# Optimization experiments

Measured on AMD Instinct MI355X. Metric: run time of the kernel, lower is better.

## Reference

```python
import jax, jax.numpy as jnp
import numpy as np
import math

B = 131072
D = 256  # latent_dim / emb_dim
MAX_T = 1000
MAX_PERIOD = 10000.0


def timestep_embedding(t, dim):
    # torch: half = dim//2; freqs = exp(-ln(max_period) * arange(half)/half)
    half = dim // 2
    freqs = jnp.exp(-math.log(MAX_PERIOD) * jnp.arange(half, dtype=jnp.float32) / half)
    args = t.astype(jnp.float32)[:, None] * freqs[None, :]  # [B, half]
    emb = jnp.concatenate([jnp.cos(args), jnp.sin(args)], axis=-1)  # [B, dim] (dim even)
    return emb


def setup_inputs() -> dict:
    key = jax.random.key(0)
    ks = jax.random.split(key, 8)
    s_emb = 0.05  # keep activations well-scaled
    x = jax.random.normal(ks[0], (B, D), jnp.float32)
    c = jax.random.normal(ks[1], (B, D), jnp.float32)
    t = jax.random.randint(ks[2], (B,), 0, MAX_T)
    # Linear weights stored torch-style as [out_features, in_features]
    W_step = jax.random.normal(ks[3], (D, D), jnp.float32) * (1.0 / math.sqrt(D))
    b_step = jnp.zeros((D,), jnp.float32)
    W1 = jax.random.normal(ks[4], (3 * D, 3 * D), jnp.float32) * math.sqrt(2.0 / (6 * D))
    b1 = jnp.zeros((3 * D,), jnp.float32)
    W2 = jax.random.normal(ks[5], (D, 3 * D), jnp.float32) * math.sqrt(2.0 / (4 * D))
    b2 = jnp.zeros((3 * D,), jnp.float32)
    del s_emb
    return {"x": x, "c": c, "t": t, "W_step": W_step, "b_step": b_step,
            "W1": W1, "b1": b1, "W2": W2, "b2": b2}


def reference(x, c, t, W_step, b_step, W1, b1, W2, b2):
    # t = step_mlp(timestep_embedding(t, D))
    t_emb = timestep_embedding(t, D) @ W_step.T + b_step           # [B, D]
    model_input = jnp.concatenate([x, c, t_emb], axis=1)           # [B, 3D]
    # diffuser: Linear(3D,3D) -> LeakyReLU(0.01) -> Linear(3D,D)
    h = jax.nn.leaky_relu(model_input @ W1.T + b1, negative_slope=0.01)
    out = h @ W2.T + b2[:D] if b2.shape[0] != D else h @ W2.T + b2
    return out
```

## Files before the change

### kernel.cpp

```cpp
#include <hip/hip_runtime.h>
#include <math.h>

#define DD    256
#define D3    768
#define KXC   512
#define MAXT  1000
#define BM    64
#define NTHR  1024
#define SMEM_BYTES 163840

using s16x8  = __attribute__((ext_vector_type(8))) short;
using f32x16 = __attribute__((ext_vector_type(16))) float;
using u16x4  = __attribute__((ext_vector_type(4))) unsigned short;

__device__ __forceinline__ unsigned short f2bf(float f) {
    union { float f; unsigned u; } v; v.f = f;
    unsigned r = v.u + 0x7fffu + ((v.u >> 16) & 1u);
    return (unsigned short)(r >> 16);
}
__device__ __forceinline__ float bf2f(unsigned short h) {
    union { unsigned u; float f; } v; v.u = ((unsigned)h) << 16;
    return v.f;
}

__global__ void k_temb(const float* __restrict__ Wstep, const float* __restrict__ bstep,
                       float* __restrict__ Temb) {
    __shared__ float emb[DD];
    const int tt  = blockIdx.x;
    const int tid = threadIdx.x;
    if (tid < 128) {
        const float nl = -9.210340371976184f;
        float f = expf(nl * (float)tid / 128.0f);
        float a = (float)tt * f;
        emb[tid]       = cosf(a);
        emb[tid + 128] = sinf(a);
    }
    __syncthreads();
    float acc = bstep[tid];
    const float* wr = Wstep + tid * DD;
    for (int k = 0; k < DD; ++k) acc = fmaf(emb[k], wr[k], acc);
    Temb[tt * DD + tid] = acc;
}

__global__ void k_t1(const float* __restrict__ Temb, const float* __restrict__ W1,
                     const float* __restrict__ b1, float* __restrict__ T1) {
    __shared__ float te[DD];
    const int tt = blockIdx.x;
    const int n  = blockIdx.y * 256 + threadIdx.x;
    te[threadIdx.x] = Temb[tt * DD + threadIdx.x];
    __syncthreads();
    float acc = b1[n];
    const float* wr = W1 + n * D3 + KXC;
    for (int k = 0; k < DD; ++k) acc = fmaf(te[k], wr[k], acc);
    T1[tt * D3 + n] = acc;
}

__global__ void k_cvtW1(const float* __restrict__ W1, unsigned short* __restrict__ hi,
                        unsigned short* __restrict__ lo) {
    int i = blockIdx.x * 256 + threadIdx.x;
    if (i >= 32 * 768 * 16) return;
    int j  = i & 7;
    int h  = (i >> 3) & 1;
    int nn = (i >> 4) % 768;
    int ks = (i >> 4) / 768;
    int k  = ks * 16 + h * 8 + j;
    float v = W1[(size_t)nn * D3 + k];
    unsigned short hh = f2bf(v);
    hi[i] = hh;
    lo[i] = f2bf(v - bf2f(hh));
}

__global__ void k_cvtW2(const float* __restrict__ W2, unsigned short* __restrict__ hi,
                        unsigned short* __restrict__ lo) {
    int i = blockIdx.x * 256 + threadIdx.x;
    if (i >= 48 * 256 * 16) return;
    int j  = i & 7;
    int h  = (i >> 3) & 1;
    int nn = (i >> 4) % 256;
    int kq = (i >> 4) / 256;
    int k  = kq * 16 + h * 8 + j;
    float v = W2[(size_t)nn * D3 + k];
    unsigned short hh = f2bf(v);
    hi[i] = hh;
    lo[i] = f2bf(v - bf2f(hh));
}

__global__ __launch_bounds__(NTHR, 4)
void k_main(const float* __restrict__ x, const float* __restrict__ c,
            const int* __restrict__ t, const float* __restrict__ T1,
            const unsigned short* __restrict__ W1hi, const unsigned short* __restrict__ W1lo,
            const unsigned short* __restrict__ W2hi, const unsigned short* __restrict__ W2lo,
            const float* __restrict__ b2, float* __restrict__ out) {
    extern __shared__ __align__(16) char smem[];
    char* Ah = smem;
    char* Al = smem + 65536;

    const int tid  = threadIdx.x;
    const int lane = tid & 63;
    const int wid  = tid >> 6;
    const int wm   = wid >> 3;
    const int wn   = wid & 7;
    const int l31  = lane & 31;
    const int lh   = lane >> 5;
    const int row0 = blockIdx.x * BM;

    const s16x8* W1hiV = (const s16x8*)W1hi;
    const s16x8* W1loV = (const s16x8*)W1lo;
    const s16x8* W2hiV = (const s16x8*)W2hi;
    const s16x8* W2loV = (const s16x8*)W2lo;

    #pragma unroll
    for (int it = 0; it < 8; ++it) {
        int q    = it * NTHR + tid;
        int row  = q >> 7;
        int col4 = q & 127;
        int k    = col4 * 4;
        const float* src = (k < 256) ? &x[(size_t)(row0 + row) * DD + k]
                                     : &c[(size_t)(row0 + row) * DD + (k - 256)];
        float4 v = *(const float4*)src;
        float f[4] = {v.x, v.y, v.z, v.w};
        u16x4 hv, lv;
        #pragma unroll
        for (int j = 0; j < 4; ++j) {
            unsigned short hh = f2bf(f[j]);
            hv[j] = hh;
            lv[j] = f2bf(f[j] - bf2f(hh));
        }
        int ks = k >> 4, h = (k >> 3) & 1, pos = k & 7;
        char* dst = Ah + ((((ks * 2 + h) * 64) + row) << 4) + pos * 2;
        *(u16x4*)dst = hv;
        *(u16x4*)(dst + 65536) = lv;
    }
    __syncthreads();

    f32x16 oacc;
    #pragma unroll
    for (int r = 0; r < 16; ++r) oacc[r] = 0.f;
    const float b2r = b2[wn * 32 + l31];

    #pragma unroll 1
    for (int p = 0; p < 3; ++p) {
        const int c0 = p * 256 + wn * 32;

        float tv[16];
        #pragma unroll
        for (int r = 0; r < 16; ++r) {
            int m = wm * 32 + (r & 3) + 8 * (r >> 2) + 4 * lh;
            tv[r] = T1[(size_t)t[row0 + m] * D3 + c0 + l31];
        }

        f32x16 acc1;
        #pragma unroll
        for (int r = 0; r < 16; ++r) acc1[r] = 0.f;

        const int nb = c0 + l31;
        const int arow = wm * 32 + l31;

        #pragma unroll 8
        for (int ks = 0; ks < 32; ++ks) {
            const s16x8 ahf = *(const s16x8*)(Ah + ((((ks * 2 + lh) * 64) + arow) << 4));
            const s16x8 alf = *(const s16x8*)(Al + ((((ks * 2 + lh) * 64) + arow) << 4));
            const s16x8 bhf = W1hiV[(ks * D3 + nb) * 2 + lh];
            const s16x8 blf = W1loV[(ks * D3 + nb) * 2 + lh];
            acc1 = __builtin_amdgcn_mfma_f32_32x32x16_bf16(alf, bhf, acc1, 0, 0, 0);
            acc1 = __builtin_amdgcn_mfma_f32_32x32x16_bf16(ahf, blf, acc1, 0, 0, 0);
            acc1 = __builtin_amdgcn_mfma_f32_32x32x16_bf16(ahf, bhf, acc1, 0, 0, 0);
        }

        #pragma unroll 1
        for (int s = 0; s < 4; ++s) {
            char* Hb = smem + 131072 + (s & 1) * 16384;
            if ((wn >> 1) == s) {
                #pragma unroll
                for (int r = 0; r < 16; ++r) {
                    int m = wm * 32 + (r & 3) + 8 * (r >> 2) + 4 * lh;
                    float v = acc1[r] + tv[r];
                    v = v > 0.f ? v : 0.01f * v;
                    unsigned short hh = f2bf(v);
                    unsigned short ll = f2bf(v - bf2f(hh));
                    int cl  = (wn & 1) * 32 + l31;
                    int kl  = cl >> 4, hb = (cl >> 3) & 1, pos = cl & 7;
                    int off = ((((kl * 2 + hb) * 64) + m) << 4) + pos * 2;
                    *(unsigned short*)(Hb + off)        = hh;
                    *(unsigned short*)(Hb + 8192 + off) = ll;
                }
            }
            __syncthreads();
            const int kq0 = p * 16 + s * 4;
            #pragma unroll
            for (int kl = 0; kl < 4; ++kl) {
                int hoff = (((kl * 2 + lh) * 64) + arow) << 4;
                const s16x8 hhf = *(const s16x8*)(Hb + hoff);
                const s16x8 hlf = *(const s16x8*)(Hb + 8192 + hoff);
                int wi = ((kq0 + kl) * DD + wn * 32 + l31) * 2 + lh;
                const s16x8 whf = W2hiV[wi];
                const s16x8 wlf = W2loV[wi];
                oacc = __builtin_amdgcn_mfma_f32_32x32x16_bf16(hlf, whf, oacc, 0, 0, 0);
                oacc = __builtin_amdgcn_mfma_f32_32x32x16_bf16(hhf, wlf, oacc, 0, 0, 0);
                oacc = __builtin_amdgcn_mfma_f32_32x32x16_bf16(hhf, whf, oacc, 0, 0, 0);
            }
        }
    }

    #pragma unroll
    for (int r = 0; r < 16; ++r) {
        int m = wm * 32 + (r & 3) + 8 * (r >> 2) + 4 * lh;
        out[(size_t)(row0 + m) * DD + wn * 32 + l31] = oacc[r] + b2r;
    }
}

extern "C" void kernel_launch(void* const* d_in, const int* in_sizes, int n_in,
                              void* d_out, int out_size, void* d_ws, size_t ws_size,
                              hipStream_t stream) {
    const float* x     = (const float*)d_in[0];
    const float* c     = (const float*)d_in[1];
    const int*   t     = (const int*)  d_in[2];
    const float* Wstep = (const float*)d_in[3];
    const float* bstep = (const float*)d_in[4];
    const float* W1    = (const float*)d_in[5];
    const float* b1    = (const float*)d_in[6];
    const float* W2    = (const float*)d_in[7];
    const float* b2    = (const float*)d_in[8];
    float*       out   = (float*)d_out;

    const int B = in_sizes[0] / DD;

    char* ws = (char*)d_ws;
    float*          Temb = (float*)(ws);
    float*          T1   = (float*)(ws + 1024000);
    unsigned short* W1hi = (unsigned short*)(ws + 4096000);
    unsigned short* W1lo = (unsigned short*)(ws + 4882432);
    unsigned short* W2hi = (unsigned short*)(ws + 5668864);
    unsigned short* W2lo = (unsigned short*)(ws + 6062080);

    k_temb<<<MAXT, 256, 0, stream>>>(Wstep, bstep, Temb);
    k_t1<<<dim3(MAXT, 3), 256, 0, stream>>>(Temb, W1, b1, T1);
    k_cvtW1<<<(32 * 768 * 16 + 255) / 256, 256, 0, stream>>>(W1, W1hi, W1lo);
    k_cvtW2<<<(48 * 256 * 16 + 255) / 256, 256, 0, stream>>>(W2, W2hi, W2lo);

    hipFuncSetAttribute((const void*)k_main, hipFuncAttributeMaxDynamicSharedMemorySize, SMEM_BYTES);
    k_main<<<B / BM, NTHR, SMEM_BYTES, stream>>>(x, c, t, T1, W1hi, W1lo, W2hi, W2lo, b2, out);
}
```

Before: 1.054 ms.

## Replace split-bf16 triple MFMA with single fp16 MFMA and retile main kernel

Drops the hi/lo bf16 split emulation, which needed three MFMAs per tile, and instead uses one fp16 MFMA per tile with fp16 weights, activations and T1 table. The block shrinks to 8 waves, each computing two 32-row M tiles so every B fragment is reused twice. LDS use drops to 80KB, and an XOR swizzle is added to avoid bank conflicts. This cuts MFMA work and memory traffic roughly threefold, at the cost of lower precision: fp16 has about 11 mantissa bits versus roughly 16 for the split scheme, and fp16 can overflow on large activations.

```diff
diff --git a/kernel.cpp b/kernel.cpp
--- a/kernel.cpp
+++ b/kernel.cpp
@@ -6,22 +6,13 @@
 #define KXC   512
 #define MAXT  1000
 #define BM    64
-#define NTHR  1024
-#define SMEM_BYTES 163840
-
-using s16x8  = __attribute__((ext_vector_type(8))) short;
+#define NTHR  512
+#define SMEM_BYTES (65536 + 16384)
+
+typedef _Float16 f16;
+using f16x8  = __attribute__((ext_vector_type(8))) _Float16;
+using f16x4  = __attribute__((ext_vector_type(4))) _Float16;
 using f32x16 = __attribute__((ext_vector_type(16))) float;
-using u16x4  = __attribute__((ext_vector_type(4))) unsigned short;
-
-__device__ __forceinline__ unsigned short f2bf(float f) {
-    union { float f; unsigned u; } v; v.f = f;
-    unsigned r = v.u + 0x7fffu + ((v.u >> 16) & 1u);
-    return (unsigned short)(r >> 16);
-}
-__device__ __forceinline__ float bf2f(unsigned short h) {
-    union { unsigned u; float f; } v; v.u = ((unsigned)h) << 16;
-    return v.f;
-}
 
 __global__ void k_temb(const float* __restrict__ Wstep, const float* __restrict__ bstep,
                        float* __restrict__ Temb) {
@@ -43,7 +34,7 @@
 }
 
 __global__ void k_t1(const float* __restrict__ Temb, const float* __restrict__ W1,
-                     const float* __restrict__ b1, float* __restrict__ T1) {
+                     const float* __restrict__ b1, f16* __restrict__ T1) {
     __shared__ float te[DD];
     const int tt = blockIdx.x;
     const int n  = blockIdx.y * 256 + threadIdx.x;
@@ -52,11 +43,10 @@
     float acc = b1[n];
     const float* wr = W1 + n * D3 + KXC;
     for (int k = 0; k < DD; ++k) acc = fmaf(te[k], wr[k], acc);
-    T1[tt * D3 + n] = acc;
-}
-
-__global__ void k_cvtW1(const float* __restrict__ W1, unsigned short* __restrict__ hi,
-                        unsigned short* __restrict__ lo) {
+    T1[tt * D3 + n] = (f16)acc;
+}
+
+__global__ void k_cvtW1(const float* __restrict__ W1, f16* __restrict__ Wf) {
     int i = blockIdx.x * 256 + threadIdx.x;
     if (i >= 32 * 768 * 16) return;
     int j  = i & 7;
@@ -64,14 +54,10 @@
     int nn = (i >> 4) % 768;
     int ks = (i >> 4) / 768;
     int k  = ks * 16 + h * 8 + j;
-    float v = W1[(size_t)nn * D3 + k];
-    unsigned short hh = f2bf(v);
-    hi[i] = hh;
-    lo[i] = f2bf(v - bf2f(hh));
-}
-
-__global__ void k_cvtW2(const float* __restrict__ W2, unsigned short* __restrict__ hi,
-                        unsigned short* __restrict__ lo) {
+    Wf[i] = (f16)W1[(size_t)nn * D3 + k];
+}
+
+__global__ void k_cvtW2(const float* __restrict__ W2, f16* __restrict__ Wf) {
     int i = blockIdx.x * 256 + threadIdx.x;
     if (i >= 48 * 256 * 16) return;
     int j  = i & 7;
@@ -79,38 +65,26 @@
     int nn = (i >> 4) % 256;
     int kq = (i >> 4) / 256;
     int k  = kq * 16 + h * 8 + j;
-    float v = W2[(size_t)nn * D3 + k];
-    unsigned short hh = f2bf(v);
-    hi[i] = hh;
-    lo[i] = f2bf(v - bf2f(hh));
+    Wf[i] = (f16)W2[(size_t)nn * D3 + k];
 }
 
 __global__ __launch_bounds__(NTHR, 4)
 void k_main(const float* __restrict__ x, const float* __restrict__ c,
-            const int* __restrict__ t, const float* __restrict__ T1,
-            const unsigned short* __restrict__ W1hi, const unsigned short* __restrict__ W1lo,
-            const unsigned short* __restrict__ W2hi, const unsigned short* __restrict__ W2lo,
+            const int* __restrict__ t, const f16* __restrict__ T1,
+            const f16* __restrict__ W1f, const f16* __restrict__ W2f,
             const float* __restrict__ b2, float* __restrict__ out) {
     extern __shared__ __align__(16) char smem[];
-    char* Ah = smem;
-    char* Al = smem + 65536;
+    char* A = smem;
 
     const int tid  = threadIdx.x;
     const int lane = tid & 63;
-    const int wid  = tid >> 6;
-    const int wm   = wid >> 3;
-    const int wn   = wid & 7;
+    const int wn   = tid >> 6;
     const int l31  = lane & 31;
     const int lh   = lane >> 5;
     const int row0 = blockIdx.x * BM;
 
-    const s16x8* W1hiV = (const s16x8*)W1hi;
-    const s16x8* W1loV = (const s16x8*)W1lo;
-    const s16x8* W2hiV = (const s16x8*)W2hi;
-    const s16x8* W2loV = (const s16x8*)W2lo;
-
     #pragma unroll
-    for (int it = 0; it < 8; ++it) {
+    for (int it = 0; it < 16; ++it) {
         int q    = it * NTHR + tid;
         int row  = q >> 7;
         int col4 = q & 127;
@@ -118,95 +92,97 @@
         const float* src = (k < 256) ? &x[(size_t)(row0 + row) * DD + k]
                                      : &c[(size_t)(row0 + row) * DD + (k - 256)];
         float4 v = *(const float4*)src;
-        float f[4] = {v.x, v.y, v.z, v.w};
-        u16x4 hv, lv;
-        #pragma unroll
-        for (int j = 0; j < 4; ++j) {
-            unsigned short hh = f2bf(f[j]);
-            hv[j] = hh;
-            lv[j] = f2bf(f[j] - bf2f(hh));
-        }
+        f16x4 hv;
+        hv[0] = (f16)v.x; hv[1] = (f16)v.y; hv[2] = (f16)v.z; hv[3] = (f16)v.w;
         int ks = k >> 4, h = (k >> 3) & 1, pos = k & 7;
-        char* dst = Ah + ((((ks * 2 + h) * 64) + row) << 4) + pos * 2;
-        *(u16x4*)dst = hv;
-        *(u16x4*)(dst + 65536) = lv;
+        int off = ((((ks * 2 + h) * 64) + row) << 4) + pos * 2;
+        off ^= (ks & 7) << 4;
+        *(f16x4*)(A + off) = hv;
     }
     __syncthreads();
 
-    f32x16 oacc;
+    f32x16 oacc[2];
     #pragma unroll
-    for (int r = 0; r < 16; ++r) oacc[r] = 0.f;
+    for (int mt = 0; mt < 2; ++mt)
+        #pragma unroll
+        for (int r = 0; r < 16; ++r) oacc[mt][r] = 0.f;
     const float b2r = b2[wn * 32 + l31];
+
+    const f16x8* W1v = (const f16x8*)W1f;
+    const f16x8* W2v = (const f16x8*)W2f;
+
+    const int s_own = wn >> 1;
+    const int nl    = (wn & 1) * 32 + l31;
 
     #pragma unroll 1
     for (int p = 0; p < 3; ++p) {
-        const int c0 = p * 256 + wn * 32;
-
-        float tv[16];
-        #pragma unroll
-        for (int r = 0; r < 16; ++r) {
-            int m = wm * 32 + (r & 3) + 8 * (r >> 2) + 4 * lh;
-            tv[r] = T1[(size_t)t[row0 + m] * D3 + c0 + l31];
-        }
-
-        f32x16 acc1;
-        #pragma unroll
-        for (int r = 0; r < 16; ++r) acc1[r] = 0.f;
-
-        const int nb = c0 + l31;
-        const int arow = wm * 32 + l31;
-
-        #pragma unroll 8
+        f16 tv[2][16];
+        #pragma unroll
+        for (int mt = 0; mt < 2; ++mt)
+            #pragma unroll
+            for (int r = 0; r < 16; ++r) {
+                int m = mt * 32 + (r & 3) + 8 * (r >> 2) + 4 * lh;
+                tv[mt][r] = T1[(size_t)t[row0 + m] * D3 + p * 256 + s_own * 64 + nl];
+            }
+
+        f32x16 acc1[2];
+        #pragma unroll
+        for (int mt = 0; mt < 2; ++mt)
+            #pragma unroll
+            for (int r = 0; r < 16; ++r) acc1[mt][r] = 0.f;
+
+        const int nb = p * 256 + wn * 32 + l31;
+
+        #pragma unroll 4
         for (int ks = 0; ks < 32; ++ks) {
-            const s16x8 ahf = *(const s16x8*)(Ah + ((((ks * 2 + lh) * 64) + arow) << 4));
-            const s16x8 alf = *(const s16x8*)(Al + ((((ks * 2 + lh) * 64) + arow) << 4));
-            const s16x8 bhf = W1hiV[(ks * D3 + nb) * 2 + lh];
-            const s16x8 blf = W1loV[(ks * D3 + nb) * 2 + lh];
-            acc1 = __builtin_amdgcn_mfma_f32_32x32x16_bf16(alf, bhf, acc1, 0, 0, 0);
-            acc1 = __builtin_amdgcn_mfma_f32_32x32x16_bf16(ahf, blf, acc1, 0, 0, 0);
-            acc1 = __builtin_amdgcn_mfma_f32_32x32x16_bf16(ahf, bhf, acc1, 0, 0, 0);
+            const f16x8 b = W1v[(ks * D3 + nb) * 2 + lh];
+            const int key = (ks & 7) << 4;
+            int off0 = ((((ks * 2 + lh) * 64) + l31) << 4) ^ key;
+            int off1 = ((((ks * 2 + lh) * 64) + 32 + l31) << 4) ^ key;
+            const f16x8 a0 = *(const f16x8*)(A + off0);
+            const f16x8 a1 = *(const f16x8*)(A + off1);
+            acc1[0] = __builtin_amdgcn_mfma_f32_32x32x16_f16(a0, b, acc1[0], 0, 0, 0);
+            acc1[1] = __builtin_amdgcn_mfma_f32_32x32x16_f16(a1, b, acc1[1], 0, 0, 0);
         }
 
         #pragma unroll 1
         for (int s = 0; s < 4; ++s) {
-            char* Hb = smem + 131072 + (s & 1) * 16384;
-            if ((wn >> 1) == s) {
+            char* Hb = smem + 65536 + (s & 1) * 8192;
+            if (s_own == s) {
                 #pragma unroll
-                for (int r = 0; r < 16; ++r) {
-                    int m = wm * 32 + (r & 3) + 8 * (r >> 2) + 4 * lh;
-                    float v = acc1[r] + tv[r];
-                    v = v > 0.f ? v : 0.01f * v;
-                    unsigned short hh = f2bf(v);
-                    unsigned short ll = f2bf(v - bf2f(hh));
-                    int cl  = (wn & 1) * 32 + l31;
-                    int kl  = cl >> 4, hb = (cl >> 3) & 1, pos = cl & 7;
-                    int off = ((((kl * 2 + hb) * 64) + m) << 4) + pos * 2;
-                    *(unsigned short*)(Hb + off)        = hh;
-                    *(unsigned short*)(Hb + 8192 + off) = ll;
-                }
+                for (int mt = 0; mt < 2; ++mt)
+                    #pragma unroll
+                    for (int r = 0; r < 16; ++r) {
+                        int m = mt * 32 + (r & 3) + 8 * (r >> 2) + 4 * lh;
+                        float v = acc1[mt][r] + (float)tv[mt][r];
+                        v = v > 0.f ? v : 0.01f * v;
+                        int off = ((m << 7) + nl * 2) ^ ((m & 7) << 4);
+                        *(f16*)(Hb + off) = (f16)v;
+                    }
             }
             __syncthreads();
             const int kq0 = p * 16 + s * 4;
             #pragma unroll
-            for (int kl = 0; kl < 4; ++kl) {
-                int hoff = (((kl * 2 + lh) * 64) + arow) << 4;
-                const s16x8 hhf = *(const s16x8*)(Hb + hoff);
-                const s16x8 hlf = *(const s16x8*)(Hb + 8192 + hoff);
-                int wi = ((kq0 + kl) * DD + wn * 32 + l31) * 2 + lh;
-                const s16x8 whf = W2hiV[wi];
-                const s16x8 wlf = W2loV[wi];
-                oacc = __builtin_amdgcn_mfma_f32_32x32x16_bf16(hlf, whf, oacc, 0, 0, 0);
-                oacc = __builtin_amdgcn_mfma_f32_32x32x16_bf16(hhf, wlf, oacc, 0, 0, 0);
-                oacc = __builtin_amdgcn_mfma_f32_32x32x16_bf16(hhf, whf, oacc, 0, 0, 0);
+            for (int q = 0; q < 4; ++q) {
+                const f16x8 w = W2v[((kq0 + q) * DD + wn * 32 + l31) * 2 + lh];
+                #pragma unroll
+                for (int mt = 0; mt < 2; ++mt) {
+                    int m = mt * 32 + l31;
+                    int off = ((m << 7) + q * 32 + lh * 16) ^ ((m & 7) << 4);
+                    const f16x8 hf = *(const f16x8*)(Hb + off);
+                    oacc[mt] = __builtin_amdgcn_mfma_f32_32x32x16_f16(hf, w, oacc[mt], 0, 0, 0);
+                }
             }
         }
     }
 
     #pragma unroll
-    for (int r = 0; r < 16; ++r) {
-        int m = wm * 32 + (r & 3) + 8 * (r >> 2) + 4 * lh;
-        out[(size_t)(row0 + m) * DD + wn * 32 + l31] = oacc[r] + b2r;
-    }
+    for (int mt = 0; mt < 2; ++mt)
+        #pragma unroll
+        for (int r = 0; r < 16; ++r) {
+            int m = mt * 32 + (r & 3) + 8 * (r >> 2) + 4 * lh;
+            out[(size_t)(row0 + m) * DD + wn * 32 + l31] = oacc[mt][r] + b2r;
+        }
 }
 
 extern "C" void kernel_launch(void* const* d_in, const int* in_sizes, int n_in,
@@ -226,18 +202,16 @@
     const int B = in_sizes[0] / DD;
 
     char* ws = (char*)d_ws;
-    float*          Temb = (float*)(ws);
-    float*          T1   = (float*)(ws + 1024000);
-    unsigned short* W1hi = (unsigned short*)(ws + 4096000);
-    unsigned short* W1lo = (unsigned short*)(ws + 4882432);
-    unsigned short* W2hi = (unsigned short*)(ws + 5668864);
-    unsigned short* W2lo = (unsigned short*)(ws + 6062080);
+    float* Temb = (float*)(ws);
+    f16*   T1   = (f16*)(ws + 1024000);
+    f16*   W1f  = (f16*)(ws + 2560000);
+    f16*   W2f  = (f16*)(ws + 3346432);
 
     k_temb<<<MAXT, 256, 0, stream>>>(Wstep, bstep, Temb);
     k_t1<<<dim3(MAXT, 3), 256, 0, stream>>>(Temb, W1, b1, T1);
-    k_cvtW1<<<(32 * 768 * 16 + 255) / 256, 256, 0, stream>>>(W1, W1hi, W1lo);
-    k_cvtW2<<<(48 * 256 * 16 + 255) / 256, 256, 0, stream>>>(W2, W2hi, W2lo);
+    k_cvtW1<<<(32 * 768 * 16 + 255) / 256, 256, 0, stream>>>(W1, W1f);
+    k_cvtW2<<<(48 * 256 * 16 + 255) / 256, 256, 0, stream>>>(W2, W2f);
 
     hipFuncSetAttribute((const void*)k_main, hipFuncAttributeMaxDynamicSharedMemorySize, SMEM_BYTES);
-    k_main<<<B / BM, NTHR, SMEM_BYTES, stream>>>(x, c, t, T1, W1hi, W1lo, W2hi, W2lo, b2, out);
-}
+    k_main<<<B / BM, NTHR, SMEM_BYTES, stream>>>(x, c, t, T1, W1f, W2f, b2, out);
+}
```

Result: faster. 957.5 us (-9.2%).
